# Optimization experiments

Hardware: AMD Instinct MI355X
Metric: run time of the kernel (lower is better)

Reference implementation:

```python
import jax, jax.numpy as jnp
import numpy as np

N = 80000    # total nodes
E = 640000   # total edges
B = 800      # graphs in batch
NPG = 100    # nodes per graph
HID = 128
NC = 10
IND = 20     # one-hot degree feature size (torch.eye(20))
EPS = 1e-5


def _gconv(x, src, dst, inv_out, inv_in, W, b):
    # DGL GraphConv, norm='both': D_out^{-1/2} scaling at src, sum-aggregate, D_in^{-1/2} at dst
    m = (x * inv_out[:, None])[src]                      # [E, F]
    agg = jax.ops.segment_sum(m, dst, num_segments=x.shape[0])
    return (agg * inv_in[:, None]) @ W + b


def _bn(x, gamma, beta):
    # BatchNorm1d, training-mode (batch statistics, biased variance)
    mu = x.mean(0)
    var = x.var(0)
    return (x - mu) / jnp.sqrt(var + EPS) * gamma + beta


def setup_inputs():
    key = jax.random.key(0)
    ks = jax.random.split(key, 10)
    # edges constrained within each graph (batched disjoint graphs, as in dgl.batch)
    eg = jax.random.randint(ks[0], (E,), 0, B)
    src = (eg * NPG + jax.random.randint(ks[1], (E,), 0, NPG)).astype(jnp.int32)
    dst = (eg * NPG + jax.random.randint(ks[2], (E,), 0, NPG)).astype(jnp.int32)
    graph_id = (jnp.arange(N) // NPG).astype(jnp.int32)

    def p(k, shape, fan):
        return (jax.random.normal(k, shape, jnp.float32) / np.sqrt(fan)).astype(jnp.float32)

    z = lambda s: jnp.zeros(s, jnp.float32)
    o = lambda s: jnp.ones(s, jnp.float32)
    return dict(
        src=src, dst=dst, graph_id=graph_id,
        W1=p(ks[3], (IND, HID), IND), b1=z((HID,)), g1=o((HID,)), be1=z((HID,)),
        W2=p(ks[4], (HID, HID), HID), b2=z((HID,)), g2=o((HID,)), be2=z((HID,)),
        Wv=p(ks[5], (HID, 1), HID), bv=z((1,)),
        Wd=p(ks[6], (1, HID), 1), bd=z((HID,)),
        Wg=p(ks[7], (HID, HID), HID), bg=z((HID,)), g3=o((HID,)), be3=z((HID,)),
        Wc=p(ks[8], (HID, NC), HID), bc=z((NC,)),
    )


def reference(src, dst, graph_id, W1, b1, g1, be1, W2, b2, g2, be2,
              Wv, bv, Wd, bd, Wg, bg, g3, be3, Wc, bc):
    n = graph_id.shape[0]
    ones_e = jnp.ones(src.shape[0], jnp.float32)
    in_deg = jax.ops.segment_sum(ones_e, dst, num_segments=n)
    out_deg = jax.ops.segment_sum(ones_e, src, num_segments=n)
    inv_in = jax.lax.rsqrt(jnp.maximum(in_deg, 1.0))   # DGL clamps deg min 1
    inv_out = jax.lax.rsqrt(jnp.maximum(out_deg, 1.0))

    # node features: one-hot of in-degree (eye(20)[in_degrees]); clip to valid range
    h = jax.nn.one_hot(jnp.clip(in_deg.astype(jnp.int32), 0, IND - 1), IND, dtype=jnp.float32)
    h = jax.nn.elu(_bn(_gconv(h, src, dst, inv_out, inv_in, W1, b1), g1, be1))  # [N,HID]
    h = jax.nn.elu(_bn(_gconv(h, src, dst, inv_out, inv_in, W2, b2), g2, be2))  # [N,HID]

    v = _gconv(h, src, dst, inv_out, inv_in, Wv, bv)   # [N,1], node weights d
    d = v[:, 0]

    # per-graph ragged matmul: vec_i = d_i^T @ h_i, done as one segment-sum
    vec = jax.ops.segment_sum(d[:, None] * h, graph_id, num_segments=B).reshape(-1)  # [B*HID]
    mean = vec.mean()
    vec = jax.nn.relu(vec - mean) - jax.nn.relu(-vec - mean)   # soft shrink by global mean

    hg = jnp.tanh(vec.reshape(B, HID))
    hg = jnp.tanh(_bn(hg @ Wg + bg, g3, be3))
    return jnp.tanh(hg @ Wc + bc)   # [B, NC] (eval-mode output)
```

## Files before the change

### kernel.cpp

```cpp
#include <hip/hip_runtime.h>
#include <hip/hip_bf16.h>
#include <math.h>

#define N_NODES 80000
#define N_EDGES 640000
#define B_GR 800
#define NPG 100
#define HID 128
#define NC 10
#define IND 20
#define BN_EPS 1e-5f

__global__ void k_A(const int* __restrict__ src, const int* __restrict__ dst,
                    unsigned int* A) {
    int e = blockIdx.x * blockDim.x + threadIdx.x;
    if (e < N_EDGES) {
        int s = src[e], d = dst[e];
        int g = d / NPG;
        int bidx = g * (NPG * NPG) + (d - g * NPG) * NPG + (s - g * NPG);
        atomicAdd(&A[bidx >> 2], 1u << ((bidx & 3) * 8));
    }
}

__global__ __launch_bounds__(128) void k_prep(const unsigned int* __restrict__ A,
                                              float* __restrict__ inv_in,
                                              float* __restrict__ inv_out,
                                              float* __restrict__ agg20) {
    __shared__ unsigned int s_A[NPG * 25];
    __shared__ float s_io[NPG];
    __shared__ int   s_ix[NPG];
    __shared__ float s_agg[NPG][IND + 1];
    int g = blockIdx.x, gbase = g * NPG, t = threadIdx.x;
    const unsigned int* Ag = A + g * 2500;
    for (int i = t; i < NPG * 25; i += 128) s_A[i] = Ag[i];
    __syncthreads();

    if (t < NPG) {
        int rsum = 0;
        const unsigned int* row = &s_A[t * 25];
#pragma unroll
        for (int q = 0; q < 25; ++q) {
            unsigned int c4 = row[q];
            rsum += (int)((c4 & 255u) + ((c4 >> 8) & 255u) + ((c4 >> 16) & 255u) + (c4 >> 24));
        }
        int csum = 0;
        int wq = t >> 2, sh = (t & 3) * 8;
#pragma unroll 4
        for (int r = 0; r < NPG; ++r)
            csum += (int)((s_A[r * 25 + wq] >> sh) & 255u);

        float io = rsqrtf(fmaxf((float)csum, 1.f));
        inv_in[gbase + t]  = rsqrtf(fmaxf((float)rsum, 1.f));
        inv_out[gbase + t] = io;
        s_io[t] = io;
        s_ix[t] = rsum > IND - 1 ? IND - 1 : rsum;
    }
    __syncthreads();

    if (t < NPG) {
#pragma unroll
        for (int k = 0; k < IND; ++k) s_agg[t][k] = 0.f;
        const unsigned int* row = &s_A[t * 25];
#pragma unroll
        for (int q = 0; q < 25; ++q) {
            unsigned int c4 = row[q];
            if (c4 == 0) continue;
#pragma unroll
            for (int b = 0; b < 4; ++b) {
                unsigned int cnt = (c4 >> (8 * b)) & 255u;
                if (cnt) {
                    int s = q * 4 + b;
                    s_agg[t][s_ix[s]] += (float)cnt * s_io[s];
                }
            }
        }
        float* outp = agg20 + (size_t)(gbase + t) * IND;
#pragma unroll
        for (int k = 0; k < IND; ++k) outp[k] = s_agg[t][k];
    }
}

#define MOM_CHUNK 64
__global__ __launch_bounds__(256) void k_mom(const float* __restrict__ agg20,
                                             const float* __restrict__ inv_in,
                                             float* s20, float* Mbuf) {
    __shared__ float rows[MOM_CHUNK * IND];
    __shared__ float w1s[MOM_CHUNK], w2s[MOM_CHUNK];
    int t = threadIdx.x;
    int k = 0, l = 0;
    bool isM = (t < 210), isS = (t >= 210 && t < 230);
    if (isM) {
        int idx = t, kk = 0;
        while (idx >= IND - kk) { idx -= IND - kk; ++kk; }
        k = kk; l = kk + idx;
    } else if (isS) {
        k = t - 210;
    }
    float acc = 0.f;
    for (int c = blockIdx.x; c < N_NODES / MOM_CHUNK; c += gridDim.x) {
        __syncthreads();
        for (int i = t * 4; i < MOM_CHUNK * IND; i += 1024)
            *(float4*)&rows[i] = *(const float4*)&agg20[(size_t)c * MOM_CHUNK * IND + i];
        if (t < MOM_CHUNK) {
            float v = inv_in[c * MOM_CHUNK + t];
            w1s[t] = v; w2s[t] = v * v;
        }
        __syncthreads();
        if (isM) {
            for (int i = 0; i < MOM_CHUNK; ++i)
                acc += w2s[i] * rows[i * IND + k] * rows[i * IND + l];
        } else if (isS) {
            for (int i = 0; i < MOM_CHUNK; ++i)
                acc += w1s[i] * rows[i * IND + k];
        }
    }
    if (isM) atomicAdd(&Mbuf[t], acc);
    else if (isS) atomicAdd(&s20[t - 210], acc);
}

__global__ void k_bn1fin(const float* __restrict__ s20, const float* __restrict__ Mbuf,
                         const float* __restrict__ W1, const float* __restrict__ b1,
                         const float* __restrict__ g1, const float* __restrict__ be1,
                         float* a1, float* c1) {
    __shared__ float sM[210], ss[IND];
    int j = threadIdx.x;
    if (j < 210) sM[j] = Mbuf[j];
    if (j + 128 < 210) sM[j + 128] = Mbuf[j + 128];
    if (j < IND) ss[j] = s20[j];
    __syncthreads();
    float w[IND];
#pragma unroll
    for (int k = 0; k < IND; ++k) w[k] = W1[k * HID + j];
    float tj = 0.f;
#pragma unroll
    for (int k = 0; k < IND; ++k) tj += ss[k] * w[k];
    float q = 0.f;
    int idx = 0;
#pragma unroll
    for (int k = 0; k < IND; ++k) {
        q += sM[idx] * w[k] * w[k]; ++idx;
#pragma unroll
        for (int l = k + 1; l < IND; ++l) { q += 2.f * sM[idx] * w[k] * w[l]; ++idx; }
    }
    float bj = b1[j];
    const float Nf = (float)N_NODES;
    float mean = (tj + Nf * bj) / Nf;
    float ey2  = (q + 2.f * bj * tj + Nf * bj * bj) / Nf;
    float var  = ey2 - mean * mean;
    float aj = g1[j] / sqrtf(var + BN_EPS);
    a1[j] = aj;
    c1[j] = be1[j] - mean * aj;
}

__global__ __launch_bounds__(256) void k_l1f(const float* __restrict__ agg20,
                                             const float* __restrict__ inv_in,
                                             const float* __restrict__ inv_out,
                                             const float* __restrict__ W1,
                                             const float* __restrict__ b1,
                                             const float* __restrict__ a1,
                                             const float* __restrict__ c1,
                                             float* __restrict__ h1s) {
    __shared__ float ws[IND * HID];
    int t = threadIdx.x;
    for (int i = t * 4; i < IND * HID; i += 1024)
        *(float4*)&ws[i] = *(const float4*)&W1[i];
    __syncthreads();
    int tx = t & 15, ty = t >> 4;
    int c0 = tx * 8;
    float4 ba = *(const float4*)(b1 + c0);
    float4 bb = *(const float4*)(b1 + c0 + 4);
    float4 aa = *(const float4*)(a1 + c0);
    float4 ab = *(const float4*)(a1 + c0 + 4);
    float4 ca = *(const float4*)(c1 + c0);
    float4 cb = *(const float4*)(c1 + c0 + 4);

    int row0 = blockIdx.x * 64 + ty * 4;
    const float* xr0 = agg20 + (size_t)row0 * IND;
    const float* xr1 = xr0 + IND;
    const float* xr2 = xr1 + IND;
    const float* xr3 = xr2 + IND;
    float acc[4][8];
#pragma unroll
    for (int r = 0; r < 4; ++r)
#pragma unroll
        for (int c = 0; c < 8; ++c) acc[r][c] = 0.f;

#pragma unroll
    for (int k = 0; k < IND; k += 4) {
        float4 x0 = *(const float4*)(xr0 + k);
        float4 x1 = *(const float4*)(xr1 + k);
        float4 x2 = *(const float4*)(xr2 + k);
        float4 x3 = *(const float4*)(xr3 + k);
#pragma unroll
        for (int kk = 0; kk < 4; ++kk) {
            float4 wa = *(const float4*)&ws[(k + kk) * HID + c0];
            float4 wb = *(const float4*)&ws[(k + kk) * HID + c0 + 4];
            float xk0 = (kk == 0) ? x0.x : (kk == 1) ? x0.y : (kk == 2) ? x0.z : x0.w;
            float xk1 = (kk == 0) ? x1.x : (kk == 1) ? x1.y : (kk == 2) ? x1.z : x1.w;
            float xk2 = (kk == 0) ? x2.x : (kk == 1) ? x2.y : (kk == 2) ? x2.z : x2.w;
            float xk3 = (kk == 0) ? x3.x : (kk == 1) ? x3.y : (kk == 2) ? x3.z : x3.w;
            acc[0][0] += xk0 * wa.x; acc[0][1] += xk0 * wa.y;
            acc[0][2] += xk0 * wa.z; acc[0][3] += xk0 * wa.w;
            acc[0][4] += xk0 * wb.x; acc[0][5] += xk0 * wb.y;
            acc[0][6] += xk0 * wb.z; acc[0][7] += xk0 * wb.w;
            acc[1][0] += xk1 * wa.x; acc[1][1] += xk1 * wa.y;
            acc[1][2] += xk1 * wa.z; acc[1][3] += xk1 * wa.w;
            acc[1][4] += xk1 * wb.x; acc[1][5] += xk1 * wb.y;
            acc[1][6] += xk1 * wb.z; acc[1][7] += xk1 * wb.w;
            acc[2][0] += xk2 * wa.x; acc[2][1] += xk2 * wa.y;
            acc[2][2] += xk2 * wa.z; acc[2][3] += xk2 * wa.w;
            acc[2][4] += xk2 * wb.x; acc[2][5] += xk2 * wb.y;
            acc[2][6] += xk2 * wb.z; acc[2][7] += xk2 * wb.w;
            acc[3][0] += xk3 * wa.x; acc[3][1] += xk3 * wa.y;
            acc[3][2] += xk3 * wa.z; acc[3][3] += xk3 * wa.w;
            acc[3][4] += xk3 * wb.x; acc[3][5] += xk3 * wb.y;
            acc[3][6] += xk3 * wb.z; acc[3][7] += xk3 * wb.w;
        }
    }
    float4 iv = *(const float4*)(inv_in + row0);
    float4 ov = *(const float4*)(inv_out + row0);
#pragma unroll
    for (int r = 0; r < 4; ++r) {
        float ivr = (r == 0) ? iv.x : (r == 1) ? iv.y : (r == 2) ? iv.z : iv.w;
        float ovr = (r == 0) ? ov.x : (r == 1) ? ov.y : (r == 2) ? ov.z : ov.w;
        float y[8];
        y[0] = acc[r][0] * ivr + ba.x; y[1] = acc[r][1] * ivr + ba.y;
        y[2] = acc[r][2] * ivr + ba.z; y[3] = acc[r][3] * ivr + ba.w;
        y[4] = acc[r][4] * ivr + bb.x; y[5] = acc[r][5] * ivr + bb.y;
        y[6] = acc[r][6] * ivr + bb.z; y[7] = acc[r][7] * ivr + bb.w;
        float z[8];
        z[0] = y[0] * aa.x + ca.x; z[1] = y[1] * aa.y + ca.y;
        z[2] = y[2] * aa.z + ca.z; z[3] = y[3] * aa.w + ca.w;
        z[4] = y[4] * ab.x + cb.x; z[5] = y[5] * ab.y + cb.y;
        z[6] = y[6] * ab.z + cb.z; z[7] = y[7] * ab.w + cb.w;
#pragma unroll
        for (int c = 0; c < 8; ++c) {
            float h = z[c] > 0.f ? z[c] : expm1f(z[c]);
            z[c] = h * ovr;
        }
        float* yr = h1s + (size_t)(row0 + r) * HID + c0;
        *(float4*)yr = make_float4(z[0], z[1], z[2], z[3]);
        *(float4*)(yr + 4) = make_float4(z[4], z[5], z[6], z[7]);
    }
}

__global__ __launch_bounds__(512) void k_agg2v5(const unsigned int* __restrict__ A,
                                                const float* __restrict__ h1s,
                                                float* __restrict__ agg2) {
    __shared__ float sh[NPG * HID];
    int t = threadIdx.x;
    int g = blockIdx.x;
    int gbase = g * NPG;

    const float4* srcp = (const float4*)(h1s + (size_t)gbase * HID);
    float4* shp = (float4*)sh;
    for (int i = t; i < (NPG * HID) / 4; i += 512)
        shp[i] = srcp[i];
    __syncthreads();

    int wv = t >> 6, lane = t & 63;
    const unsigned int* Ag = A + g * 2500;
    for (int r = wv; r < NPG; r += 8) {
        const unsigned int* row = Ag + r * 25;
        unsigned int cq[25];
#pragma unroll
        for (int q = 0; q < 25; ++q) cq[q] = row[q];
        float ax = 0.f, ay = 0.f;
#pragma unroll
        for (int q = 0; q < 25; ++q) {
            unsigned int c4 = cq[q];
            if (c4 == 0) continue;
            int sbase = q * 4;
#pragma unroll
            for (int b = 0; b < 4; ++b) {
                unsigned int cnt = (c4 >> (8 * b)) & 255u;
                if (cnt) {
                    float f = (float)cnt;
                    float2 v = *(const float2*)&sh[(sbase + b) * HID + lane * 2];
                    ax += f * v.x; ay += f * v.y;
                }
            }
        }
        *(float2*)(agg2 + (size_t)(gbase + r) * HID + lane * 2) = make_float2(ax, ay);
    }
}

__global__ void k_bnfin(const float* sums, const float* sqs,
                        const float* gamma, const float* beta,
                        float cnt, float* a, float* c) {
    int j = threadIdx.x;
    float mu  = sums[j] / cnt;
    float var = sqs[j] / cnt - mu * mu;
    float aj  = gamma[j] / sqrtf(var + BN_EPS);
    a[j] = aj;
    c[j] = beta[j] - mu * aj;
}

__global__ __launch_bounds__(512) void k_l2v5(const float* __restrict__ xin,
                                              const float* __restrict__ inv_in,
                                              const float* __restrict__ W,
                                              const float* __restrict__ bvec,
                                              float* __restrict__ yout,
                                              float* sums, float* sqs) {
    __shared__ float ws[HID * 64];
    int t = threadIdx.x;
    int tile = blockIdx.x >> 1;
    int half = blockIdx.x & 1;
    int cbase = half * 64;
    for (int i = t; i < HID * 16; i += 512) {
        int k = i >> 4;
        int c4 = (i & 15) << 2;
        *(float4*)&ws[k * 64 + c4] = *(const float4*)&W[k * HID + cbase + c4];
    }
    __syncthreads();

    int tx = t & 15;
    int ty = t >> 4;
    int c0 = tx * 4;
    float4 ba = *(const float4*)(bvec + cbase + c0);
    float csum[4], csq[4];
#pragma unroll
    for (int c = 0; c < 4; ++c) { csum[c] = 0.f; csq[c] = 0.f; }

    int row0 = tile * 128 + ty * 4;
    const float* xr0 = xin + (size_t)row0 * HID;
    const float* xr1 = xr0 + HID;
    const float* xr2 = xr1 + HID;
    const float* xr3 = xr2 + HID;
    float acc[4][4];
#pragma unroll
    for (int r = 0; r < 4; ++r)
#pragma unroll
        for (int c = 0; c < 4; ++c) acc[r][c] = 0.f;

#pragma unroll 4
    for (int k = 0; k < HID; k += 4) {
        float4 x0 = *(const float4*)(xr0 + k);
        float4 x1 = *(const float4*)(xr1 + k);
        float4 x2 = *(const float4*)(xr2 + k);
        float4 x3 = *(const float4*)(xr3 + k);
#pragma unroll
        for (int kk = 0; kk < 4; ++kk) {
            float4 wa = *(const float4*)&ws[(k + kk) * 64 + c0];
            float xk0 = (kk == 0) ? x0.x : (kk == 1) ? x0.y : (kk == 2) ? x0.z : x0.w;
            float xk1 = (kk == 0) ? x1.x : (kk == 1) ? x1.y : (kk == 2) ? x1.z : x1.w;
            float xk2 = (kk == 0) ? x2.x : (kk == 1) ? x2.y : (kk == 2) ? x2.z : x2.w;
            float xk3 = (kk == 0) ? x3.x : (kk == 1) ? x3.y : (kk == 2) ? x3.z : x3.w;
            acc[0][0] += xk0 * wa.x; acc[0][1] += xk0 * wa.y;
            acc[0][2] += xk0 * wa.z; acc[0][3] += xk0 * wa.w;
            acc[1][0] += xk1 * wa.x; acc[1][1] += xk1 * wa.y;
            acc[1][2] += xk1 * wa.z; acc[1][3] += xk1 * wa.w;
            acc[2][0] += xk2 * wa.x; acc[2][1] += xk2 * wa.y;
            acc[2][2] += xk2 * wa.z; acc[2][3] += xk2 * wa.w;
            acc[3][0] += xk3 * wa.x; acc[3][1] += xk3 * wa.y;
            acc[3][2] += xk3 * wa.z; acc[3][3] += xk3 * wa.w;
        }
    }
    float4 iv = *(const float4*)(inv_in + row0);
#pragma unroll
    for (int r = 0; r < 4; ++r) {
        float ivr = (r == 0) ? iv.x : (r == 1) ? iv.y : (r == 2) ? iv.z : iv.w;
        float y0 = acc[r][0] * ivr + ba.x;
        float y1 = acc[r][1] * ivr + ba.y;
        float y2 = acc[r][2] * ivr + ba.z;
        float y3 = acc[r][3] * ivr + ba.w;
        csum[0] += y0; csq[0] += y0 * y0;
        csum[1] += y1; csq[1] += y1 * y1;
        csum[2] += y2; csq[2] += y2 * y2;
        csum[3] += y3; csq[3] += y3 * y3;
        *(float4*)(yout + (size_t)(row0 + r) * HID + cbase + c0) = make_float4(y0, y1, y2, y3);
    }

    __syncthreads();
#pragma unroll
    for (int c = 0; c < 4; ++c) {
        ws[ty * 64 + c0 + c] = csum[c];
        ws[2048 + ty * 64 + c0 + c] = csq[c];
    }
    __syncthreads();
    if (t < 64) {
        float s1 = 0.f, s2 = 0.f;
#pragma unroll
        for (int r = 0; r < 32; ++r) {
            s1 += ws[r * 64 + t];
            s2 += ws[2048 + r * 64 + t];
        }
        atomicAdd(&sums[cbase + t], s1);
        atomicAdd(&sqs[cbase + t], s2);
    }
}

__global__ __launch_bounds__(256) void k_elu2_p(float* buf,
                                                const float* __restrict__ a,
                                                const float* __restrict__ c,
                                                const float* __restrict__ inv_out,
                                                const float* __restrict__ Wv,
                                                float* __restrict__ p) {
    int lane = threadIdx.x & 63;
    int wid = (blockIdx.x * blockDim.x + threadIdx.x) >> 6;
    int nw = (gridDim.x * blockDim.x) >> 6;
    float2 av = *(const float2*)(a + lane * 2);
    float2 cv = *(const float2*)(c + lane * 2);
    float2 wv = *(const float2*)(Wv + lane * 2);
    for (int n = wid; n < N_NODES; n += nw) {
        float2* row = (float2*)(buf + (size_t)n * HID);
        float2 x = row[lane];
        float h0 = x.x * av.x + cv.x; h0 = h0 > 0.f ? h0 : expm1f(h0);
        float h1 = x.y * av.y + cv.y; h1 = h1 > 0.f ? h1 : expm1f(h1);
        row[lane] = make_float2(h0, h1);
        float t = h0 * wv.x + h1 * wv.y;
        for (int off = 32; off; off >>= 1) t += __shfl_down(t, off);
        if (lane == 0) p[n] = t * inv_out[n];
    }
}

__global__ __launch_bounds__(128) void k_dpv2(const unsigned int* __restrict__ A,
                                              const float* __restrict__ p,
                                              const float* __restrict__ inv_in,
                                              const float* __restrict__ bv,
                                              float* __restrict__ dvec) {
    __shared__ float s_p[NPG];
    int g = blockIdx.x, gbase = g * NPG, t = threadIdx.x;
    if (t < NPG) s_p[t] = p[gbase + t];
    __syncthreads();
    if (t < NPG) {
        const unsigned int* row = A + g * 2500 + t * 25;
        unsigned int cq[25];
#pragma unroll
        for (int q = 0; q < 25; ++q) cq[q] = row[q];
        float acc = 0.f;
#pragma unroll
        for (int q = 0; q < 25; ++q) {
            unsigned int c4 = cq[q];
            if (c4 == 0) continue;
#pragma unroll
            for (int b = 0; b < 4; ++b) {
                unsigned int cnt = (c4 >> (8 * b)) & 255u;
                if (cnt) acc += (float)cnt * s_p[q * 4 + b];
            }
        }
        dvec[gbase + t] = acc * inv_in[gbase + t] + bv[0];
    }
}

__global__ __launch_bounds__(128) void k_vec(const float* __restrict__ dvec,
                                             const float* __restrict__ h2,
                                             float* vec, float* meansum) {
    __shared__ float part[2];
    int g = blockIdx.x, j = threadIdx.x;
    int base = g * NPG;
    float acc = 0.f;
    for (int i = 0; i < NPG; ++i)
        acc += dvec[base + i] * h2[(size_t)(base + i) * HID + j];
    vec[g * HID + j] = acc;
    float t = acc;
    for (int off = 32; off; off >>= 1) t += __shfl_down(t, off);
    if ((j & 63) == 0) part[j >> 6] = t;
    __syncthreads();
    if (j == 0) atomicAdd(meansum, part[0] + part[1]);
}

__global__ __launch_bounds__(128) void k_g1(const float* __restrict__ vec,
                                            const float* __restrict__ meansum,
                                            const float* __restrict__ Wg,
                                            const float* __restrict__ bg,
                                            float* y3, float* sums, float* sqs) {
    __shared__ float ws[HID * HID];
    __shared__ float rows[HID];
    int g = blockIdx.x, j = threadIdx.x;
    for (int k = 0; k < HID; ++k) ws[k * HID + j] = Wg[k * HID + j];
    float mean = meansum[0] * (1.f / (B_GR * HID));
    float v = vec[g * HID + j];
    float sh = fmaxf(v - mean, 0.f) - fmaxf(-v - mean, 0.f);
    rows[j] = tanhf(sh);
    __syncthreads();
    float acc = 0.f;
#pragma unroll 8
    for (int k = 0; k < HID; ++k) acc += rows[k] * ws[k * HID + j];
    float y = acc + bg[j];
    y3[g * HID + j] = y;
    atomicAdd(&sums[j], y);
    atomicAdd(&sqs[j], y * y);
}

__global__ __launch_bounds__(128) void k_out(const float* __restrict__ y3,
                                             const float* __restrict__ a,
                                             const float* __restrict__ c,
                                             const float* __restrict__ Wc,
                                             const float* __restrict__ bc,
                                             float* out) {
    __shared__ float hg[HID];
    int g = blockIdx.x, j = threadIdx.x;
    hg[j] = tanhf(y3[g * HID + j] * a[j] + c[j]);
    __syncthreads();
    if (j < NC) {
        float acc = 0.f;
        for (int k = 0; k < HID; ++k) acc += hg[k] * Wc[k * NC + j];
        out[g * NC + j] = tanhf(acc + bc[j]);
    }
}

extern "C" void kernel_launch(void* const* d_in, const int* in_sizes, int n_in,
                              void* d_out, int out_size, void* d_ws, size_t ws_size,
                              hipStream_t stream) {
    const int*   src = (const int*)d_in[0];
    const int*   dst = (const int*)d_in[1];
    const float* W1  = (const float*)d_in[3];
    const float* b1  = (const float*)d_in[4];
    const float* g1  = (const float*)d_in[5];
    const float* be1 = (const float*)d_in[6];
    const float* W2  = (const float*)d_in[7];
    const float* b2  = (const float*)d_in[8];
    const float* g2  = (const float*)d_in[9];
    const float* be2 = (const float*)d_in[10];
    const float* Wv  = (const float*)d_in[11];
    const float* bv  = (const float*)d_in[12];
    const float* Wg  = (const float*)d_in[15];
    const float* bg  = (const float*)d_in[16];
    const float* g3  = (const float*)d_in[17];
    const float* be3 = (const float*)d_in[18];
    const float* Wc  = (const float*)d_in[19];
    const float* bc  = (const float*)d_in[20];
    float* out = (float*)d_out;

    char* ws = (char*)d_ws;
    size_t off = 0;
    auto carve = [&](size_t bytes) -> char* {
        char* pp = ws + off;
        off = (off + bytes + 255) & ~(size_t)255;
        return pp;
    };
    unsigned int* A = (unsigned int*)carve((size_t)B_GR * NPG * NPG);
    float* stats   = (float*)carve(2048 * 4);
    size_t zbytes = off;
    float* inv_in  = (float*)carve(N_NODES * 4);
    float* inv_out = (float*)carve(N_NODES * 4);
    float* pbuf    = (float*)carve(N_NODES * 4);
    float* dvec    = (float*)carve(N_NODES * 4);
    float* vec     = (float*)carve((size_t)B_GR * HID * 4);
    float* y3      = (float*)carve((size_t)B_GR * HID * 4);
    float* agg20   = (float*)carve((size_t)N_NODES * IND * 4);
    float* bufA    = (float*)carve((size_t)N_NODES * HID * 4);
    float* bufB    = (float*)carve((size_t)N_NODES * HID * 4);

    float* sums2 = stats + 0;    float* sq2 = stats + 128;
    float* a2    = stats + 256;  float* c2  = stats + 384;
    float* sums3 = stats + 512;  float* sq3 = stats + 640;
    float* a3    = stats + 768;  float* c3  = stats + 896;
    float* meansum = stats + 1024;
    float* s20   = stats + 1056;
    float* Mbuf  = stats + 1088;
    float* a1    = stats + 1312;
    float* c1    = stats + 1440;

    hipMemsetAsync(d_ws, 0, zbytes, stream);

    k_A<<<(N_EDGES + 255) / 256, 256, 0, stream>>>(src, dst, A);
    k_prep<<<B_GR, 128, 0, stream>>>(A, inv_in, inv_out, agg20);
    k_mom<<<320, 256, 0, stream>>>(agg20, inv_in, s20, Mbuf);
    k_bn1fin<<<1, 128, 0, stream>>>(s20, Mbuf, W1, b1, g1, be1, a1, c1);
    k_l1f<<<N_NODES / 64, 256, 0, stream>>>(agg20, inv_in, inv_out, W1, b1, a1, c1, bufA);
    k_agg2v5<<<B_GR, 512, 0, stream>>>(A, bufA, bufB);
    k_l2v5<<<(N_NODES / 128) * 2, 512, 0, stream>>>(bufB, inv_in, W2, b2, bufA, sums2, sq2);
    k_bnfin<<<1, 128, 0, stream>>>(sums2, sq2, g2, be2, (float)N_NODES, a2, c2);
    k_elu2_p<<<1024, 256, 0, stream>>>(bufA, a2, c2, inv_out, Wv, pbuf);
    k_dpv2<<<B_GR, 128, 0, stream>>>(A, pbuf, inv_in, bv, dvec);
    k_vec<<<B_GR, 128, 0, stream>>>(dvec, bufA, vec, meansum);
    k_g1<<<B_GR, 128, 0, stream>>>(vec, meansum, Wg, bg, y3, sums3, sq3);
    k_bnfin<<<1, 128, 0, stream>>>(sums3, sq3, g3, be3, (float)B_GR, a3, c3);
    k_out<<<B_GR, 128, 0, stream>>>(y3, a3, c3, Wc, bc, out);
}
```

Before: 287.4 us.

## Fuse ELU, node-weight conv, and per-graph readout into one per-graph kernel

Three kernels (ELU+projection, per-graph adjacency matvec for node weights, and the per-graph weighted sum) are merged into a single kernel with one block per graph. The block stages the graph's 100x128 ELU-activated features in shared memory, computes the projection, the adjacency-weighted node weights and the readout all on-chip. This removes two launches and the write-back and re-read of the full 80000x128 activation buffer plus the intermediate p/d arrays. The cost is about 53KB of shared memory per block, which may limit occupancy.

```diff
diff --git a/kernel.cpp b/kernel.cpp
--- a/kernel.cpp
+++ b/kernel.cpp
@@ -390,39 +390,47 @@
     }
 }
 
-__global__ __launch_bounds__(256) void k_elu2_p(float* buf,
-                                                const float* __restrict__ a,
-                                                const float* __restrict__ c,
-                                                const float* __restrict__ inv_out,
-                                                const float* __restrict__ Wv,
-                                                float* __restrict__ p) {
-    int lane = threadIdx.x & 63;
-    int wid = (blockIdx.x * blockDim.x + threadIdx.x) >> 6;
-    int nw = (gridDim.x * blockDim.x) >> 6;
-    float2 av = *(const float2*)(a + lane * 2);
-    float2 cv = *(const float2*)(c + lane * 2);
-    float2 wv = *(const float2*)(Wv + lane * 2);
-    for (int n = wid; n < N_NODES; n += nw) {
-        float2* row = (float2*)(buf + (size_t)n * HID);
-        float2 x = row[lane];
-        float h0 = x.x * av.x + cv.x; h0 = h0 > 0.f ? h0 : expm1f(h0);
-        float h1 = x.y * av.y + cv.y; h1 = h1 > 0.f ? h1 : expm1f(h1);
-        row[lane] = make_float2(h0, h1);
-        float t = h0 * wv.x + h1 * wv.y;
-        for (int off = 32; off; off >>= 1) t += __shfl_down(t, off);
-        if (lane == 0) p[n] = t * inv_out[n];
-    }
-}
-
-__global__ __launch_bounds__(128) void k_dpv2(const unsigned int* __restrict__ A,
-                                              const float* __restrict__ p,
+__global__ __launch_bounds__(512) void k_post(const unsigned int* __restrict__ A,
+                                              const float* __restrict__ y2,
+                                              const float* __restrict__ a2,
+                                              const float* __restrict__ c2,
                                               const float* __restrict__ inv_in,
+                                              const float* __restrict__ inv_out,
+                                              const float* __restrict__ Wv,
                                               const float* __restrict__ bv,
-                                              float* __restrict__ dvec) {
+                                              float* __restrict__ vec,
+                                              float* meansum) {
+    __shared__ float sh[NPG * HID];
     __shared__ float s_p[NPG];
-    int g = blockIdx.x, gbase = g * NPG, t = threadIdx.x;
-    if (t < NPG) s_p[t] = p[gbase + t];
-    __syncthreads();
+    __shared__ float s_d[NPG];
+    __shared__ float s_red[512];
+    int t = threadIdx.x;
+    int g = blockIdx.x, gbase = g * NPG;
+
+    const float4* srcp = (const float4*)(y2 + (size_t)gbase * HID);
+    for (int i = t; i < (NPG * HID) / 4; i += 512) {
+        int col = (i * 4) & (HID - 1);
+        float4 v = srcp[i];
+        float4 av = *(const float4*)(a2 + col);
+        float4 cv = *(const float4*)(c2 + col);
+        float z0 = v.x * av.x + cv.x; z0 = z0 > 0.f ? z0 : expm1f(z0);
+        float z1 = v.y * av.y + cv.y; z1 = z1 > 0.f ? z1 : expm1f(z1);
+        float z2 = v.z * av.z + cv.z; z2 = z2 > 0.f ? z2 : expm1f(z2);
+        float z3 = v.w * av.w + cv.w; z3 = z3 > 0.f ? z3 : expm1f(z3);
+        *(float4*)&sh[i * 4] = make_float4(z0, z1, z2, z3);
+    }
+    __syncthreads();
+
+    int wv = t >> 6, lane = t & 63;
+    float2 wvv = *(const float2*)(Wv + lane * 2);
+    for (int r = wv; r < NPG; r += 8) {
+        float2 h = *(const float2*)&sh[r * HID + lane * 2];
+        float d = h.x * wvv.x + h.y * wvv.y;
+        for (int off = 32; off; off >>= 1) d += __shfl_down(d, off);
+        if (lane == 0) s_p[r] = d * inv_out[gbase + r];
+    }
+    __syncthreads();
+
     if (t < NPG) {
         const unsigned int* row = A + g * 2500 + t * 25;
         unsigned int cq[25];
@@ -439,25 +447,23 @@
                 if (cnt) acc += (float)cnt * s_p[q * 4 + b];
             }
         }
-        dvec[gbase + t] = acc * inv_in[gbase + t] + bv[0];
-    }
-}
-
-__global__ __launch_bounds__(128) void k_vec(const float* __restrict__ dvec,
-                                             const float* __restrict__ h2,
-                                             float* vec, float* meansum) {
-    __shared__ float part[2];
-    int g = blockIdx.x, j = threadIdx.x;
-    int base = g * NPG;
-    float acc = 0.f;
-    for (int i = 0; i < NPG; ++i)
-        acc += dvec[base + i] * h2[(size_t)(base + i) * HID + j];
-    vec[g * HID + j] = acc;
-    float t = acc;
-    for (int off = 32; off; off >>= 1) t += __shfl_down(t, off);
-    if ((j & 63) == 0) part[j >> 6] = t;
-    __syncthreads();
-    if (j == 0) atomicAdd(meansum, part[0] + part[1]);
+        s_d[t] = acc * inv_in[gbase + t] + bv[0];
+    }
+    __syncthreads();
+
+    int col = t & (HID - 1);
+    int qr = t >> 7;
+    float part = 0.f;
+    for (int r = qr * 25; r < qr * 25 + 25; ++r)
+        part += s_d[r] * sh[r * HID + col];
+    s_red[qr * HID + col] = part;
+    __syncthreads();
+    if (t < HID) {
+        float v = s_red[t] + s_red[HID + t] + s_red[2 * HID + t] + s_red[3 * HID + t];
+        vec[g * HID + t] = v;
+        for (int off = 32; off; off >>= 1) v += __shfl_down(v, off);
+        if ((t & 63) == 0) atomicAdd(meansum, v);
+    }
 }
 
 __global__ __launch_bounds__(128) void k_g1(const float* __restrict__ vec,
@@ -535,8 +541,6 @@
     size_t zbytes = off;
     float* inv_in  = (float*)carve(N_NODES * 4);
     float* inv_out = (float*)carve(N_NODES * 4);
-    float* pbuf    = (float*)carve(N_NODES * 4);
-    float* dvec    = (float*)carve(N_NODES * 4);
     float* vec     = (float*)carve((size_t)B_GR * HID * 4);
     float* y3      = (float*)carve((size_t)B_GR * HID * 4);
     float* agg20   = (float*)carve((size_t)N_NODES * IND * 4);
@@ -563,9 +567,7 @@
     k_agg2v5<<<B_GR, 512, 0, stream>>>(A, bufA, bufB);
     k_l2v5<<<(N_NODES / 128) * 2, 512, 0, stream>>>(bufB, inv_in, W2, b2, bufA, sums2, sq2);
     k_bnfin<<<1, 128, 0, stream>>>(sums2, sq2, g2, be2, (float)N_NODES, a2, c2);
-    k_elu2_p<<<1024, 256, 0, stream>>>(bufA, a2, c2, inv_out, Wv, pbuf);
-    k_dpv2<<<B_GR, 128, 0, stream>>>(A, pbuf, inv_in, bv, dvec);
-    k_vec<<<B_GR, 128, 0, stream>>>(dvec, bufA, vec, meansum);
+    k_post<<<B_GR, 512, 0, stream>>>(A, bufA, a2, c2, inv_in, inv_out, Wv, bv, vec, meansum);
     k_g1<<<B_GR, 128, 0, stream>>>(vec, meansum, Wg, bg, y3, sums3, sq3);
     k_bnfin<<<1, 128, 0, stream>>>(sums3, sq3, g3, be3, (float)B_GR, a3, c3);
     k_out<<<B_GR, 128, 0, stream>>>(y3, a3, c3, Wc, bc, out);
```

Result: no change. 284.6 us (-0.9%).
